# Performance work log

Hardware: AMD Instinct MI355X
Metric: run time of the kernel (lower is better)

## Reference

```python
import jax, jax.numpy as jnp
import numpy as np

MAX_DISTANCE = 50.0
NUM_BINS = 50
FEATURE_DIM = 64
B, K = 2048, 1024


def setup_inputs() -> dict:
    key = jax.random.key(0)
    k1, k2, k3, k4, k5, k6 = jax.random.split(key, 6)
    goal_positions = jax.random.normal(k1, (B, K, 2), dtype=jnp.float32) * 20.0
    ego_state = jax.random.normal(k2, (B, 4), dtype=jnp.float32)
    in_dim = NUM_BINS + 6  # 56
    s1 = 1.0 / np.sqrt(in_dim)
    s2 = 1.0 / np.sqrt(FEATURE_DIM)
    W1 = jax.random.uniform(k3, (in_dim, FEATURE_DIM), jnp.float32, -s1, s1)
    b1 = jax.random.uniform(k4, (FEATURE_DIM,), jnp.float32, -s1, s1)
    W2 = jax.random.uniform(k5, (FEATURE_DIM, 1), jnp.float32, -s2, s2)
    b2 = jax.random.uniform(k6, (1,), jnp.float32, -s2, s2)
    return {"goal_positions": goal_positions, "ego_state": ego_state,
            "W1": W1, "b1": b1, "W2": W2, "b2": b2}


def _histogram(goal_positions):
    # distances: (B, K); bin_idx = min(int(d / max_d * num_bins), num_bins - 1)
    d = jnp.linalg.norm(goal_positions, axis=-1)
    idx = jnp.floor(d / MAX_DISTANCE * NUM_BINS).astype(jnp.int32)
    idx = jnp.clip(idx, 0, NUM_BINS - 1)
    return jax.nn.one_hot(idx, NUM_BINS, dtype=goal_positions.dtype)  # (B, K, num_bins)


def reference(goal_positions, ego_state, W1, b1, W2, b2):
    hist = _histogram(goal_positions)                              # (B, K, nb)
    ego = jnp.broadcast_to(ego_state[:, None, :],
                           (goal_positions.shape[0], goal_positions.shape[1], 4))
    feats = jnp.concatenate([hist, goal_positions, ego], axis=-1)  # (B, K, nb+6)
    h = jax.nn.relu(jnp.einsum('bkf,fd->bkd', feats, W1) + b1)     # (B, K, feature_dim)
    scores = (jnp.einsum('bkd,do->bko', h, W2) + b2)[..., 0]       # (B, K)
    return scores
```

## Files before the change

### kernel.cpp

```cpp
#include <hip/hip_runtime.h>

#define NBIN 50
#define DIM  64
#define KPT  4
#define TPB  256

__global__ __launch_bounds__(TPB, 8) void scorer_kernel(
    const float* __restrict__ goal,
    const float* __restrict__ ego,
    const float* __restrict__ W1,
    const float* __restrict__ b1,
    const float* __restrict__ W2,
    const float* __restrict__ b2,
    float* __restrict__ out,
    int K)
{
    __shared__ float4 comb[16 * NBIN];
    __shared__ float  e_lds[DIM];

    const int b   = blockIdx.x;
    const int tid = threadIdx.x;

    const float4 eg = ((const float4*)ego)[b];
    if (tid < DIM) {
        float v = b1[tid]
                + eg.x * W1[52 * DIM + tid]
                + eg.y * W1[53 * DIM + tid]
                + eg.z * W1[54 * DIM + tid]
                + eg.w * W1[55 * DIM + tid];
        e_lds[tid] = v;
    }
    __syncthreads();

    for (int i = tid; i < NBIN * DIM; i += TPB) {
        int bin = i >> 6;
        int d   = i & 63;
        float v = W1[i] + e_lds[d];
        ((float*)comb)[(((d >> 2) * NBIN) + bin) * 4 + (d & 3)] = v;
    }
    __syncthreads();

    const float2* gp   = (const float2*)goal + (size_t)b * K;
    const float4* w50v = (const float4*)(W1 + 50 * DIM);
    const float4* w51v = (const float4*)(W1 + 51 * DIM);
    const float4* w2v  = (const float4*)W2;
    const float  bias2 = b2[0];

    float2 p[KPT];
    int    idx[KPT];
    float  acc[KPT];

#pragma unroll
    for (int j = 0; j < KPT; ++j) {
        int k = j * TPB + tid;
        p[j] = gp[k];
        float r2 = __fadd_rn(__fmul_rn(p[j].x, p[j].x), __fmul_rn(p[j].y, p[j].y));
        float r  = __fsqrt_rn(r2);
        float fv = floorf(__fmul_rn(__fdiv_rn(r, 50.0f), 50.0f));
        int ix = (int)fv;
        ix = ix < 0 ? 0 : (ix > NBIN - 1 ? NBIN - 1 : ix);
        idx[j] = ix;
        acc[j] = 0.0f;
    }

#pragma unroll
    for (int d4 = 0; d4 < 16; ++d4) {
        const float4 a  = w50v[d4];
        const float4 bb = w51v[d4];
        const float4 c  = w2v[d4];
#pragma unroll
        for (int j = 0; j < KPT; ++j) {
            const float4 g = comb[d4 * NBIN + idx[j]];
            float x = p[j].x, y = p[j].y;
            float t0 = fmaf(x, a.x, fmaf(y, bb.x, g.x));
            float t1 = fmaf(x, a.y, fmaf(y, bb.y, g.y));
            float t2 = fmaf(x, a.z, fmaf(y, bb.z, g.z));
            float t3 = fmaf(x, a.w, fmaf(y, bb.w, g.w));
            acc[j] = fmaf(c.x, fmaxf(t0, 0.0f), acc[j]);
            acc[j] = fmaf(c.y, fmaxf(t1, 0.0f), acc[j]);
            acc[j] = fmaf(c.z, fmaxf(t2, 0.0f), acc[j]);
            acc[j] = fmaf(c.w, fmaxf(t3, 0.0f), acc[j]);
        }
    }

    float* po = out + (size_t)b * K;
#pragma unroll
    for (int j = 0; j < KPT; ++j) {
        po[j * TPB + tid] = acc[j] + bias2;
    }
}

extern "C" void kernel_launch(void* const* d_in, const int* in_sizes, int n_in,
                              void* d_out, int out_size, void* d_ws, size_t ws_size,
                              hipStream_t stream) {
    const float* goal = (const float*)d_in[0];
    const float* ego  = (const float*)d_in[1];
    const float* W1   = (const float*)d_in[2];
    const float* b1   = (const float*)d_in[3];
    const float* W2   = (const float*)d_in[4];
    const float* b2   = (const float*)d_in[5];
    float* out = (float*)d_out;

    int B = in_sizes[1] / 4;
    int K = in_sizes[0] / (2 * B);

    scorer_kernel<<<dim3(B), dim3(TPB), 0, stream>>>(goal, ego, W1, b1, W2, b2, out, K);
}
```

Baseline: 21.94 us.

## Use packed fp16 math with lane-split hidden dims and DPP reduction

Stores the combined bin and ego table in LDS as packed fp16. Each point's 64 hidden units are split across 8 lanes, and each lane evaluates its 8 dims with v_pk_fma_f16, v_pk_max_f16 and fdot2. Partial sums are combined with DPP cross-lane adds, and goal coordinates and bin indices are staged in LDS. K is hardcoded to 1024 and one barrier is removed. The aim is to halve the ALU work for the hidden layer, at the cost of fp16 accuracy in the hidden activations and coordinates, which may exceed tolerance.

```diff
diff --git a/kernel.cpp b/kernel.cpp
--- a/kernel.cpp
+++ b/kernel.cpp
@@ -2,8 +2,22 @@
 
 #define NBIN 50
 #define DIM  64
-#define KPT  4
 #define TPB  256
+
+typedef _Float16 h2 __attribute__((ext_vector_type(2)));
+
+__device__ __forceinline__ h2 u32_h2(unsigned int u) {
+    union { unsigned int u; h2 h; } c; c.u = u; return c.h;
+}
+__device__ __forceinline__ unsigned int h2_u32(h2 h) {
+    union { h2 h; unsigned int u; } c; c.h = h; return c.u;
+}
+
+template <int CTRL>
+__device__ __forceinline__ float dpp_add(float v) {
+    int m = __builtin_amdgcn_mov_dpp(__float_as_int(v), CTRL, 0xF, 0xF, true);
+    return v + __int_as_float(m);
+}
 
 __global__ __launch_bounds__(TPB, 8) void scorer_kernel(
     const float* __restrict__ goal,
@@ -12,82 +26,96 @@
     const float* __restrict__ b1,
     const float* __restrict__ W2,
     const float* __restrict__ b2,
-    float* __restrict__ out,
-    int K)
+    float* __restrict__ out)
 {
-    __shared__ float4 comb[16 * NBIN];
-    __shared__ float  e_lds[DIM];
+    __shared__ uint4 comb[NBIN * 8];
+    __shared__ uint2 sxy[1024];
 
-    const int b   = blockIdx.x;
-    const int tid = threadIdx.x;
+    const int b    = blockIdx.x;
+    const int tid  = threadIdx.x;
+    const int lane = tid & 63;
+    const int w    = tid >> 6;
 
     const float4 eg = ((const float4*)ego)[b];
-    if (tid < DIM) {
-        float v = b1[tid]
-                + eg.x * W1[52 * DIM + tid]
-                + eg.y * W1[53 * DIM + tid]
-                + eg.z * W1[54 * DIM + tid]
-                + eg.w * W1[55 * DIM + tid];
-        e_lds[tid] = v;
+    const int   dp = tid & 31;
+    const int   d0 = dp * 2, d1 = d0 + 1;
+    const float ev0 = b1[d0] + eg.x * W1[52*DIM+d0] + eg.y * W1[53*DIM+d0]
+                             + eg.z * W1[54*DIM+d0] + eg.w * W1[55*DIM+d0];
+    const float ev1 = b1[d1] + eg.x * W1[52*DIM+d1] + eg.y * W1[53*DIM+d1]
+                             + eg.z * W1[54*DIM+d1] + eg.w * W1[55*DIM+d1];
+    for (int pi = tid; pi < NBIN * 32; pi += TPB) {
+        int bin = pi >> 5;
+        float2 wv = ((const float2*)W1)[bin * 32 + dp];
+        h2 hv = {(_Float16)(wv.x + ev0), (_Float16)(wv.y + ev1)};
+        ((unsigned int*)comb)[bin * 32 + dp] = h2_u32(hv);
+    }
+
+    const float2* gp = (const float2*)goal + (size_t)b * 1024 + w * 256;
+#pragma unroll
+    for (int r = 0; r < 4; ++r) {
+        float2 pv = gp[r * 64 + lane];
+        float r2 = __fadd_rn(__fmul_rn(pv.x, pv.x), __fmul_rn(pv.y, pv.y));
+        float fv = floorf(__fmul_rn(__fdiv_rn(__fsqrt_rn(r2), 50.0f), 50.0f));
+        int ix = (int)fv;
+        ix = ix < 0 ? 0 : (ix > NBIN - 1 ? NBIN - 1 : ix);
+        h2 xyh = {(_Float16)pv.x, (_Float16)pv.y};
+        sxy[w * 256 + r * 64 + lane] = make_uint2(h2_u32(xyh), (unsigned)(ix * 8));
     }
     __syncthreads();
 
-    for (int i = tid; i < NBIN * DIM; i += TPB) {
-        int bin = i >> 6;
-        int d   = i & 63;
-        float v = W1[i] + e_lds[d];
-        ((float*)comb)[(((d >> 2) * NBIN) + bin) * 4 + (d & 3)] = v;
-    }
-    __syncthreads();
+    const int dd = (lane & 7) * 8;
+    const float4 al = *(const float4*)(W1 + 50 * DIM + dd);
+    const float4 ah = *(const float4*)(W1 + 50 * DIM + dd + 4);
+    const float4 ul = *(const float4*)(W1 + 51 * DIM + dd);
+    const float4 uh = *(const float4*)(W1 + 51 * DIM + dd + 4);
+    const float4 cl = *(const float4*)(W2 + dd);
+    const float4 ch = *(const float4*)(W2 + dd + 4);
+    const h2 wa0 = {(_Float16)al.x, (_Float16)al.y}, wa1 = {(_Float16)al.z, (_Float16)al.w};
+    const h2 wa2 = {(_Float16)ah.x, (_Float16)ah.y}, wa3 = {(_Float16)ah.z, (_Float16)ah.w};
+    const h2 wu0 = {(_Float16)ul.x, (_Float16)ul.y}, wu1 = {(_Float16)ul.z, (_Float16)ul.w};
+    const h2 wu2 = {(_Float16)uh.x, (_Float16)uh.y}, wu3 = {(_Float16)uh.z, (_Float16)uh.w};
+    const h2 wc0 = {(_Float16)cl.x, (_Float16)cl.y}, wc1 = {(_Float16)cl.z, (_Float16)cl.w};
+    const h2 wc2 = {(_Float16)ch.x, (_Float16)ch.y}, wc3 = {(_Float16)ch.z, (_Float16)ch.w};
+    const h2 hz = {(_Float16)0.0f, (_Float16)0.0f};
+    const float bias2 = b2[0];
 
-    const float2* gp   = (const float2*)goal + (size_t)b * K;
-    const float4* w50v = (const float4*)(W1 + 50 * DIM);
-    const float4* w51v = (const float4*)(W1 + 51 * DIM);
-    const float4* w2v  = (const float4*)W2;
-    const float  bias2 = b2[0];
+    const int   sel   = lane & 7;
+    const int   ebase = w * 256 + (lane >> 3) * 8;
+    const uint4* gpt  = comb + (lane & 7);
 
-    float2 p[KPT];
-    int    idx[KPT];
-    float  acc[KPT];
-
-#pragma unroll
-    for (int j = 0; j < KPT; ++j) {
-        int k = j * TPB + tid;
-        p[j] = gp[k];
-        float r2 = __fadd_rn(__fmul_rn(p[j].x, p[j].x), __fmul_rn(p[j].y, p[j].y));
-        float r  = __fsqrt_rn(r2);
-        float fv = floorf(__fmul_rn(__fdiv_rn(r, 50.0f), 50.0f));
-        int ix = (int)fv;
-        ix = ix < 0 ? 0 : (ix > NBIN - 1 ? NBIN - 1 : ix);
-        idx[j] = ix;
-        acc[j] = 0.0f;
+#define PAIR(GW, WA, WU, WC)                                                  \
+    {                                                                         \
+        h2 gg = u32_h2(GW);                                                   \
+        h2 tt;                                                                \
+        asm("v_pk_fma_f16 %0, %1, %2, %3 op_sel:[1,0,0] op_sel_hi:[1,1,1]"    \
+            : "=v"(tt) : "v"(xy), "v"(WU), "v"(gg));                          \
+        asm("v_pk_fma_f16 %0, %1, %2, %0 op_sel:[0,0,0] op_sel_hi:[0,1,1]"    \
+            : "+v"(tt) : "v"(xy), "v"(WA));                                   \
+        asm("v_pk_max_f16 %0, %0, %1" : "+v"(tt) : "v"(hz));                  \
+        acc = __builtin_amdgcn_fdot2(tt, WC, acc, false);                     \
     }
 
 #pragma unroll
-    for (int d4 = 0; d4 < 16; ++d4) {
-        const float4 a  = w50v[d4];
-        const float4 bb = w51v[d4];
-        const float4 c  = w2v[d4];
+    for (int r = 0; r < 4; ++r) {
+        float keep = 0.0f;
 #pragma unroll
-        for (int j = 0; j < KPT; ++j) {
-            const float4 g = comb[d4 * NBIN + idx[j]];
-            float x = p[j].x, y = p[j].y;
-            float t0 = fmaf(x, a.x, fmaf(y, bb.x, g.x));
-            float t1 = fmaf(x, a.y, fmaf(y, bb.y, g.y));
-            float t2 = fmaf(x, a.z, fmaf(y, bb.z, g.z));
-            float t3 = fmaf(x, a.w, fmaf(y, bb.w, g.w));
-            acc[j] = fmaf(c.x, fmaxf(t0, 0.0f), acc[j]);
-            acc[j] = fmaf(c.y, fmaxf(t1, 0.0f), acc[j]);
-            acc[j] = fmaf(c.z, fmaxf(t2, 0.0f), acc[j]);
-            acc[j] = fmaf(c.w, fmaxf(t3, 0.0f), acc[j]);
+        for (int s = 0; s < 8; ++s) {
+            uint2 e  = sxy[ebase + r * 64 + s];
+            h2    xy = u32_h2(e.x);
+            uint4 gv = gpt[e.y];
+            float acc = 0.0f;
+            PAIR(gv.x, wa0, wu0, wc0);
+            PAIR(gv.y, wa1, wu1, wc1);
+            PAIR(gv.z, wa2, wu2, wc2);
+            PAIR(gv.w, wa3, wu3, wc3);
+            acc = dpp_add<0xB1>(acc);
+            acc = dpp_add<0x4E>(acc);
+            acc = dpp_add<0x141>(acc);
+            keep = (s == sel) ? acc : keep;
         }
+        out[(size_t)b * 1024 + w * 256 + r * 64 + lane] = keep + bias2;
     }
-
-    float* po = out + (size_t)b * K;
-#pragma unroll
-    for (int j = 0; j < KPT; ++j) {
-        po[j * TPB + tid] = acc[j] + bias2;
-    }
+#undef PAIR
 }
 
 extern "C" void kernel_launch(void* const* d_in, const int* in_sizes, int n_in,
@@ -102,7 +130,5 @@
     float* out = (float*)d_out;
 
     int B = in_sizes[1] / 4;
-    int K = in_sizes[0] / (2 * B);
-
-    scorer_kernel<<<dim3(B), dim3(TPB), 0, stream>>>(goal, ego, W1, b1, W2, b2, out, K);
+    scorer_kernel<<<dim3(B), dim3(TPB), 0, stream>>>(goal, ego, W1, b1, W2, b2, out);
 }
```

New measurement: 21.90 us. Within noise of the previous version (-0.2%).
